# Optimization experiments

Measured on AMD Instinct MI355X. Metric: run time of the kernel, lower is better.

## Reference

```python
import jax, jax.numpy as jnp
import numpy as np

N_NODES = 50000
N_EDGES = 640000
IN_SIZE = 512
HID1 = 128


def setup_inputs() -> dict:
    key = jax.random.key(0)
    ks = jax.random.split(key, 7)
    x = jax.random.normal(ks[0], (N_NODES, IN_SIZE), dtype=jnp.float32)
    edge_index = jax.random.randint(ks[1], (2, N_EDGES), 0, N_NODES, dtype=jnp.int64)
    # Linear params stored as (in, out) so y = x @ W + b (equiv to torch x @ W.T + b)
    s_enc = 1.0 / np.sqrt(IN_SIZE)
    s_dec = 1.0 / np.sqrt(HID1)
    W_enc = jax.random.uniform(ks[2], (IN_SIZE, HID1), jnp.float32, -s_enc, s_enc)
    b_enc = jax.random.uniform(ks[3], (HID1,), jnp.float32, -s_enc, s_enc)
    W_dec = jax.random.uniform(ks[4], (HID1, IN_SIZE), jnp.float32, -s_dec, s_dec)
    b_dec = jax.random.uniform(ks[5], (IN_SIZE,), jnp.float32, -s_dec, s_dec)
    gcn_bias = jnp.zeros((HID1,), dtype=jnp.float32)  # reset_parameters zeroes it
    return {"x": x, "W_enc": W_enc, "b_enc": b_enc, "W_dec": W_dec,
            "b_dec": b_dec, "gcn_bias": gcn_bias, "edge_index": edge_index}


def gcn_conv(h, edge_index, bias):
    # GCNConv with lin.weight frozen to identity (in==out), so lin is a no-op.
    N = h.shape[0]
    loops = jnp.arange(N, dtype=edge_index.dtype)
    row = jnp.concatenate([edge_index[0], loops])  # source nodes (x_j)
    col = jnp.concatenate([edge_index[1], loops])  # target nodes (aggregation)
    deg = jax.ops.segment_sum(jnp.ones_like(col, dtype=h.dtype), col, num_segments=N)
    dinv = jnp.where(deg > 0, jax.lax.rsqrt(deg), jnp.zeros_like(deg))
    norm = dinv[row] * dinv[col]              # [E+N]
    msg = norm[:, None] * h[row]              # gather + scale, [E+N, HID1]
    out = jax.ops.segment_sum(msg, col, num_segments=N)  # scatter-add
    return out + bias


def reference(x, W_enc, b_enc, W_dec, b_dec, gcn_bias, edge_index):
    encoded = jax.nn.relu(x @ W_enc + b_enc)          # [N, HID1]
    messaged = gcn_conv(encoded, edge_index, gcn_bias)
    decoded = jax.nn.sigmoid(messaged @ W_dec + b_dec)  # [N, IN_SIZE]
    return decoded
```

## Files before the change

### kernel.cpp

```cpp
#include <hip/hip_runtime.h>
#include <math.h>

#define NNODES 50000
#define NEDGES 640000
#define INSZ 512
#define HID 128
#define NBLK ((NNODES + 255) / 256)

typedef short s16x8 __attribute__((ext_vector_type(8)));
typedef float f32x4 __attribute__((ext_vector_type(4)));

static __device__ inline short f2bf(float f) {
    __bf16 b = (__bf16)f;
    return __builtin_bit_cast(short, b);
}

__global__ __launch_bounds__(256) void prep_wenc(const float* __restrict__ W,
                                                 short* __restrict__ WT) {
    int t = blockIdx.x * 256 + threadIdx.x;
    if (t < INSZ * HID) {
        int n = t & (HID - 1);
        int k = t >> 7;
        WT[n * INSZ + k] = f2bf(W[t]);
    }
}
__global__ __launch_bounds__(256) void prep_wdec(const float* __restrict__ W,
                                                 short* __restrict__ WT) {
    int t = blockIdx.x * 256 + threadIdx.x;
    if (t < HID * INSZ) {
        int n = t & (INSZ - 1);
        int k = t >> 9;
        WT[n * HID + k] = f2bf(W[t]);
    }
}

__global__ __launch_bounds__(256) void count_kernel(const int* __restrict__ col,
                                                    int* __restrict__ counts) {
    int e = blockIdx.x * blockDim.x + threadIdx.x;
    if (e < NEDGES) atomicAdd(&counts[col[e]], 1);
}

__global__ __launch_bounds__(256) void partial_kernel(const int* __restrict__ counts,
                                                      int* __restrict__ blocksums) {
    int i = blockIdx.x * 256 + threadIdx.x;
    int v = (i < NNODES) ? counts[i] : 0;
#pragma unroll
    for (int off = 32; off; off >>= 1) v += __shfl_down(v, off, 64);
    __shared__ int ws[4];
    if ((threadIdx.x & 63) == 0) ws[threadIdx.x >> 6] = v;
    __syncthreads();
    if (threadIdx.x == 0) blocksums[blockIdx.x] = ws[0] + ws[1] + ws[2] + ws[3];
}

__global__ __launch_bounds__(256) void scan_blocks(const int* __restrict__ blocksums,
                                                   int* __restrict__ blockoffs) {
    __shared__ int s[256];
    const int t = threadIdx.x;
    s[t] = (t < NBLK) ? blocksums[t] : 0;
    __syncthreads();
    for (int off = 1; off < 256; off <<= 1) {
        int u = (t >= off) ? s[t - off] : 0;
        __syncthreads();
        s[t] += u;
        __syncthreads();
    }
    blockoffs[t] = (t == 0) ? 0 : s[t - 1];
}

__global__ __launch_bounds__(256) void scan_final(const int* __restrict__ counts,
                                                  const int* __restrict__ blockoffs,
                                                  int* __restrict__ starts,
                                                  int* __restrict__ cursor,
                                                  float* __restrict__ dinv) {
    __shared__ int s[256];
    const int t = threadIdx.x;
    const int i = blockIdx.x * 256 + t;
    int v = (i < NNODES) ? counts[i] : 0;
    s[t] = v;
    __syncthreads();
    for (int off = 1; off < 256; off <<= 1) {
        int u = (t >= off) ? s[t - off] : 0;
        __syncthreads();
        s[t] += u;
        __syncthreads();
    }
    int excl = ((t == 0) ? 0 : s[t - 1]) + blockoffs[blockIdx.x];
    if (i < NNODES) {
        starts[i] = excl;
        cursor[i] = excl;
        dinv[i] = rsqrtf((float)v + 1.0f);
        if (i == NNODES - 1) starts[NNODES] = excl + v;
    }
}

__global__ __launch_bounds__(256) void scatter_kernel(const int* __restrict__ erow,
                                                      const int* __restrict__ ecol,
                                                      int* __restrict__ cursor,
                                                      int* __restrict__ csr_row) {
    int e = blockIdx.x * blockDim.x + threadIdx.x;
    if (e < NEDGES) {
        int pos = atomicAdd(&cursor[ecol[e]], 1);
        csr_row[pos] = erow[e];
    }
}

#define XP 520
__global__ __launch_bounds__(256) void encoder_mfma(const float* __restrict__ x,
                                                    const short* __restrict__ WT,
                                                    const float* __restrict__ b,
                                                    float* __restrict__ h) {
    __shared__ short xs[64 * XP];
    const int t    = threadIdx.x;
    const int lane = t & 63;
    const int wv   = t >> 6;
    const int r16  = lane & 15;
    const int kg   = lane >> 4;
    const int mbase = blockIdx.x * 64;
    const int nb    = wv * 32;

    for (int i = 0; i < 4; ++i) {
        float4 u[4], v[4];
#pragma unroll
        for (int j = 0; j < 4; ++j) {
            int p = (i * 4 + j) * 256 + t;
            int row = p >> 6, c8 = p & 63;
            int gr = mbase + row; if (gr >= NNODES) gr = NNODES - 1;
            const float4* src = (const float4*)(x + (size_t)gr * INSZ + c8 * 8);
            u[j] = src[0]; v[j] = src[1];
        }
#pragma unroll
        for (int j = 0; j < 4; ++j) {
            int p = (i * 4 + j) * 256 + t;
            int row = p >> 6, c8 = p & 63;
            s16x8 w;
            w[0] = f2bf(u[j].x); w[1] = f2bf(u[j].y);
            w[2] = f2bf(u[j].z); w[3] = f2bf(u[j].w);
            w[4] = f2bf(v[j].x); w[5] = f2bf(v[j].y);
            w[6] = f2bf(v[j].z); w[7] = f2bf(v[j].w);
            *(s16x8*)&xs[row * XP + c8 * 8] = w;
        }
    }
    __syncthreads();

    f32x4 acc[4][2] = {};
#pragma unroll
    for (int ks = 0; ks < 16; ++ks) {
        s16x8 a[4], bb[2];
#pragma unroll
        for (int mt = 0; mt < 4; ++mt)
            a[mt] = *(const s16x8*)&xs[(mt * 16 + r16) * XP + ks * 32 + kg * 8];
#pragma unroll
        for (int nt = 0; nt < 2; ++nt)
            bb[nt] = *(const s16x8*)(WT + (size_t)(nb + nt * 16 + r16) * INSZ + ks * 32 + kg * 8);
#pragma unroll
        for (int mt = 0; mt < 4; ++mt)
#pragma unroll
            for (int nt = 0; nt < 2; ++nt)
                acc[mt][nt] = __builtin_amdgcn_mfma_f32_16x16x32_bf16(a[mt], bb[nt], acc[mt][nt], 0, 0, 0);
    }

    const int ro = kg * 4;
#pragma unroll
    for (int mt = 0; mt < 4; ++mt) {
        const int row0 = mbase + mt * 16 + ro;
#pragma unroll
        for (int nt = 0; nt < 2; ++nt) {
            const int col = nb + nt * 16 + r16;
            const float bj = b[col];
#pragma unroll
            for (int v = 0; v < 4; ++v) {
                int rr = row0 + v;
                if (rr < NNODES)
                    h[(size_t)rr * HID + col] = fmaxf(acc[mt][nt][v] + bj, 0.0f);
            }
        }
    }
}

__global__ __launch_bounds__(256) void aggregate_csr_kernel(const int* __restrict__ starts,
                                                            const int* __restrict__ csr_row,
                                                            const float* __restrict__ dinv,
                                                            const float* __restrict__ h,
                                                            float* __restrict__ agg) {
    const int node = (blockIdx.x * 256 + threadIdx.x) >> 5;
    const int l32  = threadIdx.x & 31;
    if (node >= NNODES) return;
    const float dc = dinv[node];
    const int s0 = starts[node], s1 = starts[node + 1];
    const float4* hp = (const float4*)h;

    float4 acc = hp[(size_t)node * 32 + l32];
    const float sc = dc * dc;
    acc.x *= sc; acc.y *= sc; acc.z *= sc; acc.w *= sc;

    int i = s0;
    for (; i + 3 < s1; i += 4) {
        int r0 = csr_row[i], r1 = csr_row[i + 1], r2 = csr_row[i + 2], r3 = csr_row[i + 3];
        float n0 = dinv[r0] * dc, n1 = dinv[r1] * dc, n2 = dinv[r2] * dc, n3 = dinv[r3] * dc;
        float4 h0 = hp[(size_t)r0 * 32 + l32];
        float4 h1 = hp[(size_t)r1 * 32 + l32];
        float4 h2 = hp[(size_t)r2 * 32 + l32];
        float4 h3 = hp[(size_t)r3 * 32 + l32];
        acc.x = fmaf(n0, h0.x, acc.x); acc.y = fmaf(n0, h0.y, acc.y);
        acc.z = fmaf(n0, h0.z, acc.z); acc.w = fmaf(n0, h0.w, acc.w);
        acc.x = fmaf(n1, h1.x, acc.x); acc.y = fmaf(n1, h1.y, acc.y);
        acc.z = fmaf(n1, h1.z, acc.z); acc.w = fmaf(n1, h1.w, acc.w);
        acc.x = fmaf(n2, h2.x, acc.x); acc.y = fmaf(n2, h2.y, acc.y);
        acc.z = fmaf(n2, h2.z, acc.z); acc.w = fmaf(n2, h2.w, acc.w);
        acc.x = fmaf(n3, h3.x, acc.x); acc.y = fmaf(n3, h3.y, acc.y);
        acc.z = fmaf(n3, h3.z, acc.z); acc.w = fmaf(n3, h3.w, acc.w);
    }
    for (; i < s1; ++i) {
        int r = csr_row[i];
        float nrm = dinv[r] * dc;
        float4 hv = hp[(size_t)r * 32 + l32];
        acc.x = fmaf(nrm, hv.x, acc.x); acc.y = fmaf(nrm, hv.y, acc.y);
        acc.z = fmaf(nrm, hv.z, acc.z); acc.w = fmaf(nrm, hv.w, acc.w);
    }
    ((float4*)agg)[(size_t)node * 32 + l32] = acc;
}

#define APAD 136
#define EPAD 68
__global__ __launch_bounds__(512) void decoder_mfma(const float* __restrict__ agg,
                                                    const float* __restrict__ gb,
                                                    const short* __restrict__ WT,
                                                    const float* __restrict__ b,
                                                    float* __restrict__ out) {
    __shared__ short as_lds[64 * APAD];
    __shared__ float ep[8][16 * EPAD];
    const int t    = threadIdx.x;
    const int lane = t & 63;
    const int wv   = t >> 6;
    const int r16  = lane & 15;
    const int kg   = lane >> 4;
    const int mbase = blockIdx.x * 64;
    const int nwb   = wv * 64;

    {
        const int row = t >> 3;
        const int f0  = (t & 7) * 16;
        int gr = mbase + row; if (gr >= NNODES) gr = NNODES - 1;
        const float4* src4 = (const float4*)(agg + (size_t)gr * HID + f0);
        const float4* g4   = (const float4*)(gb + f0);
        short4* d4 = (short4*)(as_lds + row * APAD + f0);
#pragma unroll
        for (int j = 0; j < 4; ++j) {
            float4 u = src4[j], g = g4[j];
            short4 w;
            w.x = f2bf(u.x + g.x); w.y = f2bf(u.y + g.y);
            w.z = f2bf(u.z + g.z); w.w = f2bf(u.w + g.w);
            d4[j] = w;
        }
    }
    __syncthreads();

    f32x4 acc[4][4] = {};
#pragma unroll
    for (int ks = 0; ks < 4; ++ks) {
        s16x8 a[4], bb[4];
#pragma unroll
        for (int mt = 0; mt < 4; ++mt)
            a[mt] = *(const s16x8*)&as_lds[(mt * 16 + r16) * APAD + ks * 32 + kg * 8];
#pragma unroll
        for (int nt = 0; nt < 4; ++nt)
            bb[nt] = *(const s16x8*)(WT + (size_t)(nwb + nt * 16 + r16) * HID + ks * 32 + kg * 8);
#pragma unroll
        for (int mt = 0; mt < 4; ++mt)
#pragma unroll
            for (int nt = 0; nt < 4; ++nt)
                acc[mt][nt] = __builtin_amdgcn_mfma_f32_16x16x32_bf16(a[mt], bb[nt], acc[mt][nt], 0, 0, 0);
    }

    float bj[4];
#pragma unroll
    for (int nt = 0; nt < 4; ++nt) bj[nt] = b[nwb + nt * 16 + r16];

    float* eps = ep[wv];
#pragma unroll
    for (int mt = 0; mt < 4; ++mt) {
#pragma unroll
        for (int nt = 0; nt < 4; ++nt)
#pragma unroll
            for (int v = 0; v < 4; ++v) {
                float z = acc[mt][nt][v] + bj[nt];
                eps[(kg * 4 + v) * EPAD + nt * 16 + r16] = 1.0f / (1.0f + __expf(-z));
            }
#pragma unroll
        for (int pass = 0; pass < 4; ++pass) {
            const int lr = pass * 4 + kg;
            float4 vv = *(const float4*)&eps[lr * EPAD + r16 * 4];
            const int rr = mbase + mt * 16 + lr;
            if (rr < NNODES)
                *(float4*)&out[(size_t)rr * INSZ + nwb + r16 * 4] = vv;
        }
    }
}

extern "C" void kernel_launch(void* const* d_in, const int* in_sizes, int n_in,
                              void* d_out, int out_size, void* d_ws, size_t ws_size,
                              hipStream_t stream) {
    const float* x        = (const float*)d_in[0];
    const float* W_enc    = (const float*)d_in[1];
    const float* b_enc    = (const float*)d_in[2];
    const float* W_dec    = (const float*)d_in[3];
    const float* b_dec    = (const float*)d_in[4];
    const float* gcn_bias = (const float*)d_in[5];
    const int*   edge     = (const int*)d_in[6];
    const int*   erow = edge;
    const int*   ecol = edge + NEDGES;

    float* out = (float*)d_out;
    float* agg   = (float*)d_ws;
    float* dinv  = agg + (size_t)NNODES * HID;
    short* wdecT = (short*)(dinv + NNODES);
    float* h         = out;
    int*   csr_row   = (int*)(out + (size_t)NNODES * HID);
    int*   starts    = csr_row + NEDGES;
    int*   counts    = starts + NNODES + 1;
    int*   cursor    = counts + NNODES;
    int*   blocksums = cursor + NNODES;
    int*   blockoffs = blocksums + 256;
    short* wencT     = (short*)(blockoffs + 256);

    hipMemsetAsync(counts, 0, (size_t)NNODES * sizeof(int), stream);
    prep_wenc<<<(INSZ * HID + 255) / 256, 256, 0, stream>>>(W_enc, wencT);
    prep_wdec<<<(HID * INSZ + 255) / 256, 256, 0, stream>>>(W_dec, wdecT);
    count_kernel<<<(NEDGES + 255) / 256, 256, 0, stream>>>(ecol, counts);
    partial_kernel<<<NBLK, 256, 0, stream>>>(counts, blocksums);
    scan_blocks<<<1, 256, 0, stream>>>(blocksums, blockoffs);
    scan_final<<<NBLK, 256, 0, stream>>>(counts, blockoffs, starts, cursor, dinv);
    scatter_kernel<<<(NEDGES + 255) / 256, 256, 0, stream>>>(erow, ecol, cursor, csr_row);
    encoder_mfma<<<(NNODES + 63) / 64, 256, 0, stream>>>(x, wencT, b_enc, h);
    aggregate_csr_kernel<<<((size_t)NNODES * 32 + 255) / 256, 256, 0, stream>>>(starts, csr_row, dinv, h, agg);
    decoder_mfma<<<(NNODES + 63) / 64, 512, 0, stream>>>(agg, gcn_bias, wdecT, b_dec, out);
}
```

Measured before the change: 214.9 us.

## Drop shared-memory staging in encoder; keep x rows in registers

The encoder GEMM no longer stages a 64x512 bf16 tile of x in LDS. Each wave now loads its own 16 rows of x straight into registers as MFMA A operands and computes all 128 output columns. B fragments of the transposed weight are double-buffered from global memory across k-steps. This removes the LDS round trip and the block barrier, and lowers LDS use so more blocks fit per CU. In exchange it raises register pressure (16 A fragments plus 16 B fragments per lane) and makes each wave read the whole weight matrix from cache.

```diff
diff --git a/kernel.cpp b/kernel.cpp
--- a/kernel.cpp
+++ b/kernel.cpp
@@ -104,75 +104,77 @@
     }
 }
 
-#define XP 520
-__global__ __launch_bounds__(256) void encoder_mfma(const float* __restrict__ x,
-                                                    const short* __restrict__ WT,
-                                                    const float* __restrict__ b,
-                                                    float* __restrict__ h) {
-    __shared__ short xs[64 * XP];
-    const int t    = threadIdx.x;
-    const int lane = t & 63;
-    const int wv   = t >> 6;
+__global__ __launch_bounds__(256, 2) void encoder_mfma(const float* __restrict__ x,
+                                                       const short* __restrict__ WT,
+                                                       const float* __restrict__ b,
+                                                       float* __restrict__ h) {
+    const int lane = threadIdx.x & 63;
+    const int wv   = threadIdx.x >> 6;
     const int r16  = lane & 15;
     const int kg   = lane >> 4;
-    const int mbase = blockIdx.x * 64;
-    const int nb    = wv * 32;
-
-    for (int i = 0; i < 4; ++i) {
-        float4 u[4], v[4];
-#pragma unroll
-        for (int j = 0; j < 4; ++j) {
-            int p = (i * 4 + j) * 256 + t;
-            int row = p >> 6, c8 = p & 63;
-            int gr = mbase + row; if (gr >= NNODES) gr = NNODES - 1;
-            const float4* src = (const float4*)(x + (size_t)gr * INSZ + c8 * 8);
-            u[j] = src[0]; v[j] = src[1];
-        }
-#pragma unroll
-        for (int j = 0; j < 4; ++j) {
-            int p = (i * 4 + j) * 256 + t;
-            int row = p >> 6, c8 = p & 63;
+    const int rowbase = blockIdx.x * 64 + wv * 16;
+
+    int gr = rowbase + r16;
+    if (gr >= NNODES) gr = NNODES - 1;
+    const float* xrow = x + (size_t)gr * INSZ + kg * 8;
+
+    s16x8 A[16];
+#pragma unroll
+    for (int half = 0; half < 2; ++half) {
+        float4 u[8], v[8];
+#pragma unroll
+        for (int i = 0; i < 8; ++i) {
+            const float* p = xrow + (half * 8 + i) * 32;
+            u[i] = *(const float4*)p;
+            v[i] = *(const float4*)(p + 4);
+        }
+#pragma unroll
+        for (int i = 0; i < 8; ++i) {
             s16x8 w;
-            w[0] = f2bf(u[j].x); w[1] = f2bf(u[j].y);
-            w[2] = f2bf(u[j].z); w[3] = f2bf(u[j].w);
-            w[4] = f2bf(v[j].x); w[5] = f2bf(v[j].y);
-            w[6] = f2bf(v[j].z); w[7] = f2bf(v[j].w);
-            *(s16x8*)&xs[row * XP + c8 * 8] = w;
-        }
-    }
-    __syncthreads();
-
-    f32x4 acc[4][2] = {};
+            w[0] = f2bf(u[i].x); w[1] = f2bf(u[i].y);
+            w[2] = f2bf(u[i].z); w[3] = f2bf(u[i].w);
+            w[4] = f2bf(v[i].x); w[5] = f2bf(v[i].y);
+            w[6] = f2bf(v[i].z); w[7] = f2bf(v[i].w);
+            A[half * 8 + i] = w;
+        }
+    }
+
+    const short* wbase = WT + (size_t)r16 * INSZ + kg * 8;
+    f32x4 acc[8] = {};
+    s16x8 B0[8], B1[8];
+#pragma unroll
+    for (int nt = 0; nt < 8; ++nt)
+        B0[nt] = *(const s16x8*)(wbase + nt * 16 * INSZ);
 #pragma unroll
     for (int ks = 0; ks < 16; ++ks) {
-        s16x8 a[4], bb[2];
-#pragma unroll
-        for (int mt = 0; mt < 4; ++mt)
-            a[mt] = *(const s16x8*)&xs[(mt * 16 + r16) * XP + ks * 32 + kg * 8];
-#pragma unroll
-        for (int nt = 0; nt < 2; ++nt)
-            bb[nt] = *(const s16x8*)(WT + (size_t)(nb + nt * 16 + r16) * INSZ + ks * 32 + kg * 8);
-#pragma unroll
-        for (int mt = 0; mt < 4; ++mt)
-#pragma unroll
-            for (int nt = 0; nt < 2; ++nt)
-                acc[mt][nt] = __builtin_amdgcn_mfma_f32_16x16x32_bf16(a[mt], bb[nt], acc[mt][nt], 0, 0, 0);
-    }
-
-    const int ro = kg * 4;
-#pragma unroll
-    for (int mt = 0; mt < 4; ++mt) {
-        const int row0 = mbase + mt * 16 + ro;
-#pragma unroll
-        for (int nt = 0; nt < 2; ++nt) {
-            const int col = nb + nt * 16 + r16;
-            const float bj = b[col];
-#pragma unroll
-            for (int v = 0; v < 4; ++v) {
-                int rr = row0 + v;
-                if (rr < NNODES)
-                    h[(size_t)rr * HID + col] = fmaxf(acc[mt][nt][v] + bj, 0.0f);
+        if (ks & 1) {
+            if (ks < 15) {
+#pragma unroll
+                for (int nt = 0; nt < 8; ++nt)
+                    B0[nt] = *(const s16x8*)(wbase + nt * 16 * INSZ + (ks + 1) * 32);
             }
+#pragma unroll
+            for (int nt = 0; nt < 8; ++nt)
+                acc[nt] = __builtin_amdgcn_mfma_f32_16x16x32_bf16(A[ks], B1[nt], acc[nt], 0, 0, 0);
+        } else {
+#pragma unroll
+            for (int nt = 0; nt < 8; ++nt)
+                B1[nt] = *(const s16x8*)(wbase + nt * 16 * INSZ + (ks + 1) * 32);
+#pragma unroll
+            for (int nt = 0; nt < 8; ++nt)
+                acc[nt] = __builtin_amdgcn_mfma_f32_16x16x32_bf16(A[ks], B0[nt], acc[nt], 0, 0, 0);
+        }
+    }
+
+#pragma unroll
+    for (int nt = 0; nt < 8; ++nt) {
+        const int col = nt * 16 + r16;
+        const float bj = b[col];
+#pragma unroll
+        for (int v = 0; v < 4; ++v) {
+            int rr = rowbase + kg * 4 + v;
+            if (rr < NNODES)
+                h[(size_t)rr * HID + col] = fmaxf(acc[nt][v] + bj, 0.0f);
         }
     }
 }
```

New measurement: 252.7 us. 17.6% more time.
